# Kernel optimization log

Measured on AMD Instinct MI355X. Metric: run time of the kernel, lower is better.

## Reference

```python
import jax, jax.numpy as jnp
import numpy as np

NEG_SLOPE = 0.01


def _pos(x):
    return jnp.where(x > 0, x, jnp.zeros_like(x))


def _neg(x):
    return jnp.where(x < 0, x, jnp.zeros_like(x))


def setup_inputs() -> dict:
    N = 4096
    key = jax.random.key(0)
    k1, k2, k3, k4, k5, k6 = jax.random.split(key, 6)
    x = jax.random.normal(k1, (1, N), dtype=jnp.float32)
    eps = 0.1
    lb0 = x - eps
    ub0 = x + eps
    scale = 1.0 / np.sqrt(N)
    W1 = jax.random.normal(k2, (N, N), dtype=jnp.float32) * scale
    b1 = jax.random.normal(k3, (1, N), dtype=jnp.float32)
    W2 = jax.random.normal(k4, (N, N), dtype=jnp.float32) * scale
    b2 = jax.random.normal(k5, (1, N), dtype=jnp.float32)
    raw_alpha = jax.random.normal(k6, (N,), dtype=jnp.float32)
    return {"lb0": lb0, "ub0": ub0, "W1": W1, "b1": b1, "W2": W2, "b2": b2, "raw_alpha": raw_alpha}


def reference(lb0, ub0, W1, b1, W2, b2, raw_alpha):
    N = raw_alpha.shape[0]
    ns = NEG_SLOPE
    # ---- backsubstitution: fold layer2 transformer through layer1 (affine: lslope=uslope=W1) ----
    clslope, clintercept, cuslope, cuintercept = W2, b2, W2, b2
    clp, cln = _pos(clslope), _neg(clslope)
    cup, cun = _pos(cuslope), _neg(cuslope)
    clintercept = b1 @ clp.T + b1 @ cln.T + clintercept  # [1,N]
    cuintercept = b1 @ cup.T + b1 @ cun.T + cuintercept
    clslope = clp @ W1 + cln @ W1  # [N,N]
    cuslope = cup @ W1 + cun @ W1
    # ---- certifier against initial interval bounds ----
    lsp, lsn = _pos(clslope), _neg(clslope)
    usp, usn = _pos(cuslope), _neg(cuslope)
    lbounds = lb0 @ lsp.T + ub0 @ lsn.T + clintercept  # [1,N]
    ubounds = ub0 @ usp.T + lb0 @ usn.T + cuintercept
    # ---- DeepPoly LeakyReLU relaxation (neg_slope <= 1 branch) ----
    alpha = jax.nn.sigmoid(raw_alpha)
    slope = ((ubounds - lbounds * ns) / (ubounds - lbounds)).reshape(-1)  # [N]
    slope = jnp.where(jnp.isnan(slope), jnp.zeros_like(slope), slope)
    intercept = (1.0 - slope) * ubounds  # [1,N]
    ones = jnp.ones((N,), dtype=lbounds.dtype)
    zeros_row = jnp.zeros((1, N), dtype=lbounds.dtype)
    lslope, lintercept = ones, zeros_row
    uslope, uintercept = ones, zeros_row
    below = (ubounds <= 0).reshape(-1)
    above = (lbounds >= 0).reshape(-1)
    lslope = jnp.where(below, ns * ones, lslope)
    uslope = jnp.where(below, ns * ones, uslope)
    lslope = jnp.where(above, ones, lslope)
    uslope = jnp.where(above, ones, uslope)
    crossing = ~(below | above)
    uslope = jnp.where(crossing, slope, uslope)
    uintercept = jnp.where(crossing, intercept, uintercept)
    lslope_v1 = jnp.where(crossing, ones, lslope)
    lslope_v2 = jnp.where(crossing, ns * ones, lslope)
    lslope = alpha * lslope_v1 + (1.0 - alpha) * lslope_v2
    return jnp.diag(lslope), lintercept, jnp.diag(uslope), uintercept
```

## Files before the change

### kernel.cpp

```cpp
#include <hip/hip_runtime.h>
#include <stdint.h>

#define NN 4096
#define NEG_SLOPE 0.01f

typedef _Float16 f16x8 __attribute__((ext_vector_type(8)));
typedef _Float16 f16x4 __attribute__((ext_vector_type(4)));
typedef float f32x4 __attribute__((ext_vector_type(4)));

#define L_INT  16777216
#define U_DIAG 16781312
#define U_INT  33558528
#define TAIL0  33554432
#define TAIL2  33554432

__device__ __forceinline__ void async_ld16(void* lds, const void* g) {
    __builtin_amdgcn_global_load_lds(
        (__attribute__((address_space(1))) const void*)(const void*)g,
        (__attribute__((address_space(3))) void*)lds, 16, 0, 0);
}

template<int EVERY>
__global__ __launch_bounds__(256, 4)
void gemm_SU(const _Float16* __restrict__ Ah, const _Float16* __restrict__ Bt,
             const float* __restrict__ lb0, const float* __restrict__ ub0,
             float* __restrict__ S, float* __restrict__ U,
             f32x4* __restrict__ zbase) {
    __shared__ _Float16 sA[128][64];
    __shared__ _Float16 sB[128][64];
    const int t = threadIdx.x;
    const int lane = t & 63;
    const int w = t >> 6;
    const int waveRow = w >> 1, waveCol = w & 1;
    const int quad = lane >> 4, l15 = lane & 15, l7 = lane & 7;

    const int bRow = (blockIdx.x >> 5) * 128;
    const int bCol = (blockIdx.x & 31) * 128;

    const int rOff = lane >> 3;
    const int uG   = (lane & 7) ^ (lane >> 3);
    const _Float16* gA = Ah + (size_t)(bRow + w * 32 + rOff) * NN + uG * 8;
    const _Float16* gB = Bt + (size_t)(bCol + w * 32 + rOff) * NN + uG * 8;

    f32x4 acc[4][4];
#pragma unroll
    for (int i = 0; i < 4; ++i)
#pragma unroll
        for (int j = 0; j < 4; ++j) acc[i][j] = (f32x4){0.f, 0.f, 0.f, 0.f};

    const f32x4 zv = (f32x4){0.f, 0.f, 0.f, 0.f};
    const int NZB = (64 / EVERY) * 256;

    for (int kt = 0; kt < NN / 64; ++kt) {
        const int k0 = kt * 64;
        __syncthreads();
#pragma unroll
        for (int i = 0; i < 4; ++i) {
            async_ld16(&sA[w * 32 + i * 8][0], gA + (size_t)(i * 8) * NN + k0);
            async_ld16(&sB[w * 32 + i * 8][0], gB + (size_t)(i * 8) * NN + k0);
        }
        __syncthreads();

#pragma unroll
        for (int s = 0; s < 2; ++s) {
            f16x8 af[4];
#pragma unroll
            for (int fr = 0; fr < 4; ++fr) {
                const int r = waveRow * 64 + fr * 16 + l15;
                af[fr] = *(const f16x8*)&sA[r][((s * 4 + quad) ^ l7) * 8];
            }
#pragma unroll
            for (int fc = 0; fc < 4; ++fc) {
                const int c = waveCol * 64 + fc * 16 + l15;
                const f16x8 bf = *(const f16x8*)&sB[c][((s * 4 + quad) ^ l7) * 8];
#pragma unroll
                for (int fr = 0; fr < 4; ++fr)
                    acc[fr][fc] = __builtin_amdgcn_mfma_f32_16x16x32_f16(af[fr], bf, acc[fr][fc], 0, 0, 0);
            }
        }

        if ((kt & (EVERY - 1)) == 0) {
            const int zi = kt / EVERY;
            __builtin_nontemporal_store(zv,
                zbase + (size_t)blockIdx.x * NZB + zi * 256 + t);
        }
    }

    float ev[4], cv[4];
#pragma unroll
    for (int fc = 0; fc < 4; ++fc) {
        const int col = bCol + waveCol * 64 + fc * 16 + l15;
        const float l = lb0[col], u_ = ub0[col];
        ev[fc] = 0.5f * (u_ - l);
        cv[fc] = 0.5f * (u_ + l);
    }
#pragma unroll
    for (int fr = 0; fr < 4; ++fr) {
#pragma unroll
        for (int r = 0; r < 4; ++r) {
            float sv = 0.f, uv = 0.f;
#pragma unroll
            for (int fc = 0; fc < 4; ++fc) {
                const float m = acc[fr][fc][r];
                sv += ev[fc] * fabsf(m);
                uv += cv[fc] * m;
            }
#pragma unroll
            for (int mk = 1; mk < 16; mk <<= 1) {
                sv += __shfl_xor(sv, mk, 64);
                uv += __shfl_xor(uv, mk, 64);
            }
            if (l15 == 0) {
                const int row = bRow + waveRow * 64 + fr * 16 + quad * 4 + r;
                atomicAdd(&S[row], sv);
                atomicAdd(&U[row], uv);
            }
        }
    }
}

__global__ __launch_bounds__(256)
void prep_a(const float* __restrict__ W2, const float* __restrict__ b1,
            const float* __restrict__ b2, _Float16* __restrict__ Ah,
            float* __restrict__ cj, float* __restrict__ S, float* __restrict__ U) {
    const int lane = threadIdx.x & 63;
    const int w = threadIdx.x >> 6;
    const int j = blockIdx.x * 4 + w;
    const float* row = W2 + (size_t)j * NN;
    _Float16* orow = Ah + (size_t)j * NN;
    float d1 = 0.f;
#pragma unroll
    for (int q = 0; q < 8; ++q) {
        const int i = q * 512 + lane * 8;
        const float4 a0 = *(const float4*)&row[i];
        const float4 a1 = *(const float4*)&row[i + 4];
        const float4 c0 = *(const float4*)&b1[i];
        const float4 c1 = *(const float4*)&b1[i + 4];
        d1 += a0.x * c0.x + a0.y * c0.y + a0.z * c0.z + a0.w * c0.w;
        d1 += a1.x * c1.x + a1.y * c1.y + a1.z * c1.z + a1.w * c1.w;
        f16x8 h;
        h[0] = (_Float16)a0.x; h[1] = (_Float16)a0.y;
        h[2] = (_Float16)a0.z; h[3] = (_Float16)a0.w;
        h[4] = (_Float16)a1.x; h[5] = (_Float16)a1.y;
        h[6] = (_Float16)a1.z; h[7] = (_Float16)a1.w;
        *(f16x8*)&orow[i] = h;
    }
#pragma unroll
    for (int mk = 1; mk < 64; mk <<= 1) d1 += __shfl_xor(d1, mk, 64);
    if (lane == 0) {
        cj[j] = d1 + b2[j];
        S[j] = 0.f;
        U[j] = 0.f;
    }
}

__global__ __launch_bounds__(256)
void prep_t(const float* __restrict__ W1, _Float16* __restrict__ Bt) {
    __shared__ float sT[64][65];
    const int t = threadIdx.x;
    const int tile = blockIdx.x;
    const int bi = (tile & 63) * 64;
    const int bn = (tile >> 6) * 64;
    const int r = t >> 4, c4 = (t & 15) * 4;
#pragma unroll
    for (int p = 0; p < 4; ++p) {
        const float4 a = *(const float4*)&W1[(size_t)(bi + r + p * 16) * NN + bn + c4];
        sT[r + p * 16][c4 + 0] = a.x;
        sT[r + p * 16][c4 + 1] = a.y;
        sT[r + p * 16][c4 + 2] = a.z;
        sT[r + p * 16][c4 + 3] = a.w;
    }
    __syncthreads();
    const int k8 = (t & 7) * 8;
#pragma unroll
    for (int p = 0; p < 2; ++p) {
        const int n = (t >> 3) + p * 32;
        f16x8 h;
#pragma unroll
        for (int e = 0; e < 8; ++e) h[e] = (_Float16)sT[k8 + e][n];
        *(f16x8*)&Bt[(size_t)(bn + n) * NN + bi + k8] = h;
    }
}

__device__ __forceinline__ void get_lub(int j, const float* S, const float* U,
                                        const float* cj, float& lb, float& ub) {
    const float base = U[j] + cj[j], Sv = S[j];
    lb = base - Sv;
    ub = base + Sv;
}
__device__ __forceinline__ float slope_of(float lb, float ub) {
    float s = (ub - lb * NEG_SLOPE) / (ub - lb);
    if (!(s == s)) s = 0.f;
    return s;
}
__device__ __forceinline__ float uslope_of(float lb, float ub) {
    const bool below = (ub <= 0.f), above = (lb >= 0.f);
    return (!(below || above)) ? slope_of(lb, ub) : (below ? NEG_SLOPE : 1.f);
}
__device__ __forceinline__ float lslope_of(float lb, float ub, float raw) {
    const float alpha = 1.f / (1.f + expf(-raw));
    const bool below = (ub <= 0.f), above = (lb >= 0.f);
    const bool crossing = !(below || above);
    const float v1 = below ? NEG_SLOPE : 1.f;
    const float v2 = crossing ? NEG_SLOPE : v1;
    return alpha * v1 + (1.f - alpha) * v2;
}

__global__ __launch_bounds__(256)
void finish_fast(const float* __restrict__ S, const float* __restrict__ U,
                 const float* __restrict__ cj, const float* __restrict__ ra,
                 float* __restrict__ out) {
    const int b = blockIdx.x;
    const int t = threadIdx.x;
    if (b == 0) {
        f32x4* p = (f32x4*)(out + TAIL2);
#pragma unroll
        for (int q = 0; q < 4; ++q) {
            const int i4 = t + q * 256;
            f32x4 z = (f32x4){0.f, 0.f, 0.f, 0.f};
            if (i4 == 1023) {
                float lb, ub;
                get_lub(4095, S, U, cj, lb, ub);
                z[3] = uslope_of(lb, ub);
            }
            __builtin_nontemporal_store(z, &p[i4]);
        }
    } else if (b <= 16) {
        const int j = (b - 1) * 256 + t;
        float lb, ub;
        get_lub(j, S, U, cj, lb, ub);
        out[(size_t)j * (NN + 1)] = lslope_of(lb, ub, ra[j]);
        if (j < 4095)
            out[U_DIAG + (size_t)j * (NN + 1)] = uslope_of(lb, ub);
    } else {
#pragma unroll
        for (int q = 0; q < 16; ++q) {
            const int j = t + q * 256;
            float lb, ub;
            get_lub(j, S, U, cj, lb, ub);
            const bool below = (ub <= 0.f), above = (lb >= 0.f);
            const bool crossing = !(below || above);
            out[U_INT + j] = crossing ? (1.f - slope_of(lb, ub)) * ub : 0.f;
        }
    }
}

__global__ __launch_bounds__(256)
void finish_slow(const float* __restrict__ S, const float* __restrict__ U,
                 const float* __restrict__ cj, const float* __restrict__ ra,
                 float* __restrict__ out) {
    const int b = blockIdx.x;
    const int t = threadIdx.x;
    if (b < 4096) {
        const int j = b;
        float lb, ub;
        get_lub(j, S, U, cj, lb, ub);
        const float ls = lslope_of(lb, ub, ra[j]);
        f32x4* rowp = (f32x4*)(out + (size_t)j * NN);
        const int dq = j >> 2, dr = j & 3;
#pragma unroll
        for (int q = 0; q < 4; ++q) {
            const int i4 = t + q * 256;
            f32x4 z = (f32x4){0.f, 0.f, 0.f, 0.f};
            if (i4 == dq) z[dr] = ls;
            __builtin_nontemporal_store(z, &rowp[i4]);
        }
    } else if (b < 4112) {
        const int j = (b - 4096) * 256 + t;
        if (j < 4095) {
            float lb, ub;
            get_lub(j, S, U, cj, lb, ub);
            out[U_DIAG + (size_t)j * NN + j] = uslope_of(lb, ub);
        }
    } else if (b == 4112) {
        f32x4* p = (f32x4*)(out + TAIL0);
#pragma unroll
        for (int q = 0; q < 4; ++q) {
            const int i4 = t + q * 256;
            f32x4 z = (f32x4){0.f, 0.f, 0.f, 0.f};
            if (i4 == 1023) {
                float lb, ub;
                get_lub(4095, S, U, cj, lb, ub);
                z[3] = uslope_of(lb, ub);
            }
            __builtin_nontemporal_store(z, &p[i4]);
        }
    } else {
#pragma unroll
        for (int q = 0; q < 16; ++q) {
            const int j = t + q * 256;
            float lb, ub;
            get_lub(j, S, U, cj, lb, ub);
            const bool below = (ub <= 0.f), above = (lb >= 0.f);
            const bool crossing = !(below || above);
            out[U_INT + j] = crossing ? (1.f - slope_of(lb, ub)) * ub : 0.f;
        }
    }
}

extern "C" void kernel_launch(void* const* d_in, const int* in_sizes, int n_in,
                              void* d_out, int out_size, void* d_ws, size_t ws_size,
                              hipStream_t stream) {
    const float* lb0 = (const float*)d_in[0];
    const float* ub0 = (const float*)d_in[1];
    const float* W1  = (const float*)d_in[2];
    const float* b1  = (const float*)d_in[3];
    const float* W2  = (const float*)d_in[4];
    const float* b2  = (const float*)d_in[5];
    const float* ra  = (const float*)d_in[6];
    float* out = (float*)d_out;

    float* S  = (float*)d_ws;
    float* U  = S + NN;
    float* cj = U + NN;

    const size_t need = 3 * (size_t)NN * sizeof(float)
                      + 2 * (size_t)NN * NN * sizeof(_Float16);
    const bool fast = ws_size >= need;

    if (fast) {
        _Float16* Ah = (_Float16*)(cj + NN);
        _Float16* Bt = Ah + (size_t)NN * NN;
        prep_a<<<dim3(1024), dim3(256), 0, stream>>>(W2, b1, b2, Ah, cj, S, U);
        prep_t<<<dim3(4096), dim3(256), 0, stream>>>(W1, Bt);
        gemm_SU<2><<<dim3(1024), dim3(256), 0, stream>>>(Ah, Bt, lb0, ub0, S, U,
                                                         (f32x4*)out);
        finish_fast<<<dim3(18), dim3(256), 0, stream>>>(S, U, cj, ra, out);
    } else {
        _Float16* Ah = (_Float16*)d_out;
        _Float16* Bt = Ah + (size_t)NN * NN;
        prep_a<<<dim3(1024), dim3(256), 0, stream>>>(W2, b1, b2, Ah, cj, S, U);
        prep_t<<<dim3(4096), dim3(256), 0, stream>>>(W1, Bt);
        gemm_SU<4><<<dim3(1024), dim3(256), 0, stream>>>(Ah, Bt, lb0, ub0, S, U,
                                                         (f32x4*)(out + L_INT));
        finish_slow<<<dim3(4114), dim3(256), 0, stream>>>(S, U, cj, ra, out);
    }
}
```

Baseline: 377.0 us.

## Merge prep kernels and fold finish step into GEMM via last-block counter

Combines the two preprocessing kernels (W2 fp16 conversion with bias dot, and W1 transpose-convert) into one launch, and removes the separate finish kernel on the fast path. The GEMM now uses an atomic completion counter so the last block to finish writes the diagonal slopes, tail zeros and upper intercepts. This removes two kernel launches and their gaps, at the cost of one serial block doing the finish work and an extra threadfence and atomic in every GEMM block.

```diff
diff --git a/kernel.cpp b/kernel.cpp
--- a/kernel.cpp
+++ b/kernel.cpp
@@ -5,7 +5,6 @@
 #define NEG_SLOPE 0.01f
 
 typedef _Float16 f16x8 __attribute__((ext_vector_type(8)));
-typedef _Float16 f16x4 __attribute__((ext_vector_type(4)));
 typedef float f32x4 __attribute__((ext_vector_type(4)));
 
 #define L_INT  16777216
@@ -20,12 +19,38 @@
         (__attribute__((address_space(3))) void*)lds, 16, 0, 0);
 }
 
-template<int EVERY>
+__device__ __forceinline__ void get_lub(int j, const float* S, const float* U,
+                                        const float* cj, float& lb, float& ub) {
+    const float base = U[j] + cj[j], Sv = S[j];
+    lb = base - Sv;
+    ub = base + Sv;
+}
+__device__ __forceinline__ float slope_of(float lb, float ub) {
+    float s = (ub - lb * NEG_SLOPE) / (ub - lb);
+    if (!(s == s)) s = 0.f;
+    return s;
+}
+__device__ __forceinline__ float uslope_of(float lb, float ub) {
+    const bool below = (ub <= 0.f), above = (lb >= 0.f);
+    return (!(below || above)) ? slope_of(lb, ub) : (below ? NEG_SLOPE : 1.f);
+}
+__device__ __forceinline__ float lslope_of(float lb, float ub, float raw) {
+    const float alpha = 1.f / (1.f + expf(-raw));
+    const bool below = (ub <= 0.f), above = (lb >= 0.f);
+    const bool crossing = !(below || above);
+    const float v1 = below ? NEG_SLOPE : 1.f;
+    const float v2 = crossing ? NEG_SLOPE : v1;
+    return alpha * v1 + (1.f - alpha) * v2;
+}
+
+template<int EVERY, bool FIN>
 __global__ __launch_bounds__(256, 4)
 void gemm_SU(const _Float16* __restrict__ Ah, const _Float16* __restrict__ Bt,
              const float* __restrict__ lb0, const float* __restrict__ ub0,
              float* __restrict__ S, float* __restrict__ U,
-             f32x4* __restrict__ zbase) {
+             const float* __restrict__ cj, const float* __restrict__ ra,
+             float* __restrict__ out, f32x4* __restrict__ zbase,
+             int* __restrict__ done) {
     __shared__ _Float16 sA[128][64];
     __shared__ _Float16 sB[128][64];
     const int t = threadIdx.x;
@@ -117,130 +142,113 @@
             }
         }
     }
+
+    if (FIN) {
+        __shared__ int lastFlag;
+        __threadfence();
+        __syncthreads();
+        if (t == 0) lastFlag = (atomicAdd(done, 1) == (int)gridDim.x - 1);
+        __syncthreads();
+        if (lastFlag) {
+            __threadfence();
+            {
+                f32x4* p = (f32x4*)(out + TAIL2);
+#pragma unroll
+                for (int q = 0; q < 4; ++q) {
+                    const int i4 = t + q * 256;
+                    f32x4 z = (f32x4){0.f, 0.f, 0.f, 0.f};
+                    if (i4 == 1023) {
+                        float lb, ub;
+                        get_lub(4095, S, U, cj, lb, ub);
+                        z[3] = uslope_of(lb, ub);
+                    }
+                    __builtin_nontemporal_store(z, &p[i4]);
+                }
+            }
+#pragma unroll 1
+            for (int q = 0; q < 16; ++q) {
+                const int j = q * 256 + t;
+                float lb, ub;
+                get_lub(j, S, U, cj, lb, ub);
+                out[(size_t)j * (NN + 1)] = lslope_of(lb, ub, ra[j]);
+                if (j < 4095)
+                    out[U_DIAG + (size_t)j * (NN + 1)] = uslope_of(lb, ub);
+            }
+#pragma unroll 1
+            for (int q = 0; q < 16; ++q) {
+                const int j = t + q * 256;
+                float lb, ub;
+                get_lub(j, S, U, cj, lb, ub);
+                const bool below = (ub <= 0.f), above = (lb >= 0.f);
+                const bool crossing = !(below || above);
+                out[U_INT + j] = crossing ? (1.f - slope_of(lb, ub)) * ub : 0.f;
+            }
+        }
+    }
 }
 
 __global__ __launch_bounds__(256)
-void prep_a(const float* __restrict__ W2, const float* __restrict__ b1,
-            const float* __restrict__ b2, _Float16* __restrict__ Ah,
-            float* __restrict__ cj, float* __restrict__ S, float* __restrict__ U) {
-    const int lane = threadIdx.x & 63;
-    const int w = threadIdx.x >> 6;
-    const int j = blockIdx.x * 4 + w;
-    const float* row = W2 + (size_t)j * NN;
-    _Float16* orow = Ah + (size_t)j * NN;
-    float d1 = 0.f;
-#pragma unroll
-    for (int q = 0; q < 8; ++q) {
-        const int i = q * 512 + lane * 8;
-        const float4 a0 = *(const float4*)&row[i];
-        const float4 a1 = *(const float4*)&row[i + 4];
-        const float4 c0 = *(const float4*)&b1[i];
-        const float4 c1 = *(const float4*)&b1[i + 4];
-        d1 += a0.x * c0.x + a0.y * c0.y + a0.z * c0.z + a0.w * c0.w;
-        d1 += a1.x * c1.x + a1.y * c1.y + a1.z * c1.z + a1.w * c1.w;
-        f16x8 h;
-        h[0] = (_Float16)a0.x; h[1] = (_Float16)a0.y;
-        h[2] = (_Float16)a0.z; h[3] = (_Float16)a0.w;
-        h[4] = (_Float16)a1.x; h[5] = (_Float16)a1.y;
-        h[6] = (_Float16)a1.z; h[7] = (_Float16)a1.w;
-        *(f16x8*)&orow[i] = h;
-    }
-#pragma unroll
-    for (int mk = 1; mk < 64; mk <<= 1) d1 += __shfl_xor(d1, mk, 64);
-    if (lane == 0) {
-        cj[j] = d1 + b2[j];
-        S[j] = 0.f;
-        U[j] = 0.f;
-    }
-}
-
-__global__ __launch_bounds__(256)
-void prep_t(const float* __restrict__ W1, _Float16* __restrict__ Bt) {
+void prep(const float* __restrict__ W2, const float* __restrict__ W1,
+          const float* __restrict__ b1, const float* __restrict__ b2,
+          _Float16* __restrict__ Ah, _Float16* __restrict__ Bt,
+          float* __restrict__ cj, float* __restrict__ S, float* __restrict__ U,
+          int* __restrict__ done) {
     __shared__ float sT[64][65];
-    const int t = threadIdx.x;
-    const int tile = blockIdx.x;
-    const int bi = (tile & 63) * 64;
-    const int bn = (tile >> 6) * 64;
-    const int r = t >> 4, c4 = (t & 15) * 4;
-#pragma unroll
-    for (int p = 0; p < 4; ++p) {
-        const float4 a = *(const float4*)&W1[(size_t)(bi + r + p * 16) * NN + bn + c4];
-        sT[r + p * 16][c4 + 0] = a.x;
-        sT[r + p * 16][c4 + 1] = a.y;
-        sT[r + p * 16][c4 + 2] = a.z;
-        sT[r + p * 16][c4 + 3] = a.w;
-    }
-    __syncthreads();
-    const int k8 = (t & 7) * 8;
-#pragma unroll
-    for (int p = 0; p < 2; ++p) {
-        const int n = (t >> 3) + p * 32;
-        f16x8 h;
-#pragma unroll
-        for (int e = 0; e < 8; ++e) h[e] = (_Float16)sT[k8 + e][n];
-        *(f16x8*)&Bt[(size_t)(bn + n) * NN + bi + k8] = h;
-    }
-}
-
-__device__ __forceinline__ void get_lub(int j, const float* S, const float* U,
-                                        const float* cj, float& lb, float& ub) {
-    const float base = U[j] + cj[j], Sv = S[j];
-    lb = base - Sv;
-    ub = base + Sv;
-}
-__device__ __forceinline__ float slope_of(float lb, float ub) {
-    float s = (ub - lb * NEG_SLOPE) / (ub - lb);
-    if (!(s == s)) s = 0.f;
-    return s;
-}
-__device__ __forceinline__ float uslope_of(float lb, float ub) {
-    const bool below = (ub <= 0.f), above = (lb >= 0.f);
-    return (!(below || above)) ? slope_of(lb, ub) : (below ? NEG_SLOPE : 1.f);
-}
-__device__ __forceinline__ float lslope_of(float lb, float ub, float raw) {
-    const float alpha = 1.f / (1.f + expf(-raw));
-    const bool below = (ub <= 0.f), above = (lb >= 0.f);
-    const bool crossing = !(below || above);
-    const float v1 = below ? NEG_SLOPE : 1.f;
-    const float v2 = crossing ? NEG_SLOPE : v1;
-    return alpha * v1 + (1.f - alpha) * v2;
-}
-
-__global__ __launch_bounds__(256)
-void finish_fast(const float* __restrict__ S, const float* __restrict__ U,
-                 const float* __restrict__ cj, const float* __restrict__ ra,
-                 float* __restrict__ out) {
     const int b = blockIdx.x;
     const int t = threadIdx.x;
-    if (b == 0) {
-        f32x4* p = (f32x4*)(out + TAIL2);
-#pragma unroll
-        for (int q = 0; q < 4; ++q) {
-            const int i4 = t + q * 256;
-            f32x4 z = (f32x4){0.f, 0.f, 0.f, 0.f};
-            if (i4 == 1023) {
-                float lb, ub;
-                get_lub(4095, S, U, cj, lb, ub);
-                z[3] = uslope_of(lb, ub);
-            }
-            __builtin_nontemporal_store(z, &p[i4]);
-        }
-    } else if (b <= 16) {
-        const int j = (b - 1) * 256 + t;
-        float lb, ub;
-        get_lub(j, S, U, cj, lb, ub);
-        out[(size_t)j * (NN + 1)] = lslope_of(lb, ub, ra[j]);
-        if (j < 4095)
-            out[U_DIAG + (size_t)j * (NN + 1)] = uslope_of(lb, ub);
+    if (b < 1024) {
+        if (b == 0 && t == 0) *done = 0;
+        const int lane = t & 63;
+        const int w = t >> 6;
+        const int j = b * 4 + w;
+        const float* row = W2 + (size_t)j * NN;
+        _Float16* orow = Ah + (size_t)j * NN;
+        float d1 = 0.f;
+#pragma unroll
+        for (int q = 0; q < 8; ++q) {
+            const int i = q * 512 + lane * 8;
+            const float4 a0 = *(const float4*)&row[i];
+            const float4 a1 = *(const float4*)&row[i + 4];
+            const float4 c0 = *(const float4*)&b1[i];
+            const float4 c1 = *(const float4*)&b1[i + 4];
+            d1 += a0.x * c0.x + a0.y * c0.y + a0.z * c0.z + a0.w * c0.w;
+            d1 += a1.x * c1.x + a1.y * c1.y + a1.z * c1.z + a1.w * c1.w;
+            f16x8 h;
+            h[0] = (_Float16)a0.x; h[1] = (_Float16)a0.y;
+            h[2] = (_Float16)a0.z; h[3] = (_Float16)a0.w;
+            h[4] = (_Float16)a1.x; h[5] = (_Float16)a1.y;
+            h[6] = (_Float16)a1.z; h[7] = (_Float16)a1.w;
+            *(f16x8*)&orow[i] = h;
+        }
+#pragma unroll
+        for (int mk = 1; mk < 64; mk <<= 1) d1 += __shfl_xor(d1, mk, 64);
+        if (lane == 0) {
+            cj[j] = d1 + b2[j];
+            S[j] = 0.f;
+            U[j] = 0.f;
+        }
     } else {
-#pragma unroll
-        for (int q = 0; q < 16; ++q) {
-            const int j = t + q * 256;
-            float lb, ub;
-            get_lub(j, S, U, cj, lb, ub);
-            const bool below = (ub <= 0.f), above = (lb >= 0.f);
-            const bool crossing = !(below || above);
-            out[U_INT + j] = crossing ? (1.f - slope_of(lb, ub)) * ub : 0.f;
+        const int tile = b - 1024;
+        const int bi = (tile & 63) * 64;
+        const int bn = (tile >> 6) * 64;
+        const int r = t >> 4, c4 = (t & 15) * 4;
+#pragma unroll
+        for (int p = 0; p < 4; ++p) {
+            const float4 a = *(const float4*)&W1[(size_t)(bi + r + p * 16) * NN + bn + c4];
+            sT[r + p * 16][c4 + 0] = a.x;
+            sT[r + p * 16][c4 + 1] = a.y;
+            sT[r + p * 16][c4 + 2] = a.z;
+            sT[r + p * 16][c4 + 3] = a.w;
+        }
+        __syncthreads();
+        const int k8 = (t & 7) * 8;
+#pragma unroll
+        for (int p = 0; p < 2; ++p) {
+            const int n = (t >> 3) + p * 32;
+            f16x8 h;
+#pragma unroll
+            for (int e = 0; e < 8; ++e) h[e] = (_Float16)sT[k8 + e][n];
+            *(f16x8*)&Bt[(size_t)(bn + n) * NN + bi + k8] = h;
         }
     }
 }
@@ -310,29 +318,29 @@
     const float* ra  = (const float*)d_in[6];
     float* out = (float*)d_out;
 
-    float* S  = (float*)d_ws;
-    float* U  = S + NN;
-    float* cj = U + NN;
-
-    const size_t need = 3 * (size_t)NN * sizeof(float)
+    float* S   = (float*)d_ws;
+    float* U   = S + NN;
+    float* cj  = U + NN;
+    int*  done = (int*)(cj + NN);
+
+    const size_t need = (3 * (size_t)NN + 4) * sizeof(float)
                       + 2 * (size_t)NN * NN * sizeof(_Float16);
     const bool fast = ws_size >= need;
 
     if (fast) {
-        _Float16* Ah = (_Float16*)(cj + NN);
+        _Float16* Ah = (_Float16*)((float*)d_ws + 3 * NN + 4);
         _Float16* Bt = Ah + (size_t)NN * NN;
-        prep_a<<<dim3(1024), dim3(256), 0, stream>>>(W2, b1, b2, Ah, cj, S, U);
-        prep_t<<<dim3(4096), dim3(256), 0, stream>>>(W1, Bt);
-        gemm_SU<2><<<dim3(1024), dim3(256), 0, stream>>>(Ah, Bt, lb0, ub0, S, U,
-                                                         (f32x4*)out);
-        finish_fast<<<dim3(18), dim3(256), 0, stream>>>(S, U, cj, ra, out);
+        prep<<<dim3(5120), dim3(256), 0, stream>>>(W2, W1, b1, b2, Ah, Bt,
+                                                   cj, S, U, done);
+        gemm_SU<2, true><<<dim3(1024), dim3(256), 0, stream>>>(
+            Ah, Bt, lb0, ub0, S, U, cj, ra, out, (f32x4*)out, done);
     } else {
         _Float16* Ah = (_Float16*)d_out;
         _Float16* Bt = Ah + (size_t)NN * NN;
-        prep_a<<<dim3(1024), dim3(256), 0, stream>>>(W2, b1, b2, Ah, cj, S, U);
-        prep_t<<<dim3(4096), dim3(256), 0, stream>>>(W1, Bt);
-        gemm_SU<4><<<dim3(1024), dim3(256), 0, stream>>>(Ah, Bt, lb0, ub0, S, U,
-                                                         (f32x4*)(out + L_INT));
+        prep<<<dim3(5120), dim3(256), 0, stream>>>(W2, W1, b1, b2, Ah, Bt,
+                                                   cj, S, U, done);
+        gemm_SU<4, false><<<dim3(1024), dim3(256), 0, stream>>>(
+            Ah, Bt, lb0, ub0, S, U, cj, ra, out, (f32x4*)(out + L_INT), done);
         finish_slow<<<dim3(4114), dim3(256), 0, stream>>>(S, U, cj, ra, out);
     }
 }
```

Result: slower. 515.1 us (+36.6%).
